# Optimization experiments

Measured on AMD Instinct MI355X. Metric: run time of the kernel, lower is better.

## Reference

```python
import jax, jax.numpy as jnp
import numpy as np

NEG_SLOPE = 0.1

def lrelu(x):
    return jnp.where(x >= 0, x, NEG_SLOPE * x)

def conv1d(x, w, b, stride=2):
    # x: [N, C_in, W], w: [C_out, C_in, K], VALID padding, given stride
    y = jax.lax.conv_general_dilated(x, w, (stride,), 'VALID',
                                     dimension_numbers=('NCH', 'OIH', 'NCH'))
    return y + b[None, :, None]

def setup_inputs() -> dict:
    key = jax.random.key(0)
    ks = jax.random.split(key, 16)
    N_NODES = 50000
    N_EDGES = 4950000
    POS_C, CONV_C, CONV_W = 3, 3, 151
    HID, OUT = 256, 1
    W2 = 37  # width after two stride-2 k=3 convs on 151
    IN_G = POS_C + W2  # 40

    def lin_init(k, fan_out, fan_in):
        s = 1.0 / np.sqrt(fan_in)
        k1, k2 = jax.random.split(k)
        return (jax.random.uniform(k1, (fan_out, fan_in), jnp.float32, -s, s),
                jax.random.uniform(k2, (fan_out,), jnp.float32, -s, s))

    pose = jax.random.normal(ks[0], (N_NODES, POS_C), jnp.float32)
    views = jax.random.normal(ks[1], (N_NODES, CONV_C, CONV_W), jnp.float32)
    edge_index = jax.random.randint(ks[2], (2, N_EDGES), 0, N_NODES, jnp.int64)

    # encoder1: Conv1d(3 -> 9, k=3, s=2); encoder2: Conv1d(9 -> 1, k=3, s=2)
    s1 = 1.0 / np.sqrt(CONV_C * 3)
    w_e1 = jax.random.uniform(ks[3], (CONV_C ** 2, CONV_C, 3), jnp.float32, -s1, s1)
    b_e1 = jax.random.uniform(ks[4], (CONV_C ** 2,), jnp.float32, -s1, s1)
    s2 = 1.0 / np.sqrt(CONV_C ** 2 * 3)
    w_e2 = jax.random.uniform(ks[5], (1, CONV_C ** 2, 3), jnp.float32, -s2, s2)
    b_e2 = jax.random.uniform(ks[6], (1,), jnp.float32, -s2, s2)

    # GraphConv: lin_rel (with bias) on aggregated neighbors, lin_root (no bias) on self
    w_rel, b_rel = lin_init(ks[7], HID, IN_G)
    w_root, _ = lin_init(ks[8], HID, IN_G)

    w_l1, b_l1 = lin_init(ks[9], HID, HID)
    w_l2, b_l2 = lin_init(ks[10], HID, HID)
    w_l3, b_l3 = lin_init(ks[11], HID, HID)
    w_pred, b_pred = lin_init(ks[12], OUT, HID)

    return dict(pose=pose, views=views, edge_index=edge_index,
                w_e1=w_e1, b_e1=b_e1, w_e2=w_e2, b_e2=b_e2,
                w_rel=w_rel, b_rel=b_rel, w_root=w_root,
                w_l1=w_l1, b_l1=b_l1, w_l2=w_l2, b_l2=b_l2,
                w_l3=w_l3, b_l3=b_l3, w_pred=w_pred, b_pred=b_pred)

def reference(pose, views, edge_index, w_e1, b_e1, w_e2, b_e2,
              w_rel, b_rel, w_root,
              w_l1, b_l1, w_l2, b_l2, w_l3, b_l3, w_pred, b_pred):
    n_nodes = pose.shape[0]
    # view encoder
    v = lrelu(conv1d(views, w_e1, b_e1))          # [N, 9, 75]
    v = lrelu(conv1d(v, w_e2, b_e2))              # [N, 1, 37]
    x = jnp.concatenate([pose, v[:, 0, :]], axis=1)  # [N, 40]
    # GraphConv (aggr='add'): out = lin_rel(sum_{j->i} x_j) + lin_root(x_i)
    src, dst = edge_index[0], edge_index[1]
    agg = jax.ops.segment_sum(x[src], dst, num_segments=n_nodes)  # [N, 40]
    h = lrelu(agg @ w_rel.T + b_rel + x @ w_root.T)               # [N, 256]
    # MLP stack (dropout is identity in eval mode)
    h = lrelu(h @ w_l1.T + b_l1)
    h = lrelu(h @ w_l2.T + b_l2)
    h = lrelu(h @ w_l3.T + b_l3)
    return h @ w_pred.T + b_pred  # [N, 1]
```

## Files before the change

### kernel.cpp

```cpp
#include <hip/hip_runtime.h>
#include <hip/hip_fp16.h>

#define NEG_SLOPE 0.1f
__device__ __forceinline__ float lrelu(float v) { return fmaxf(v, NEG_SLOPE * v); }

constexpr int CAP = 8704;
constexpr int EPB = 8192;

typedef __attribute__((ext_vector_type(8))) short short8;
typedef __attribute__((ext_vector_type(4))) float f32x4;

__device__ __forceinline__ unsigned short f2bf(float f) {
    union { float f; unsigned u; } v; v.f = f;
    const unsigned r = v.u + 0x7FFF + ((v.u >> 16) & 1);
    return (unsigned short)(r >> 16);
}
__device__ __forceinline__ float bf2f(unsigned short h) {
    union { unsigned u; float f; } v; v.u = ((unsigned)h) << 16;
    return v.f;
}

__global__ __launch_bounds__(256) void encoder_kernel(
        const float* __restrict__ pose,
        const float* __restrict__ views,
        const float* __restrict__ w1, const float* __restrict__ b1,
        const float* __restrict__ w2, const float* __restrict__ b2,
        const float* __restrict__ w_l1, const float* __restrict__ w_l2,
        const float* __restrict__ w_l3, const float* __restrict__ w_rel,
        const float* __restrict__ w_root,
        unsigned short* __restrict__ Wb1, unsigned short* __restrict__ Wb2,
        unsigned short* __restrict__ Wb3, unsigned short* __restrict__ Wg,
        int* __restrict__ gcur,
        unsigned short* __restrict__ xHi, unsigned short* __restrict__ xLo,
        __half* __restrict__ xh, int N)
{
    __shared__ float s_w1[81];
    __shared__ float s_b1[9];
    __shared__ float s_w2[27];
    __shared__ float s_b2[1];
    __shared__ float s_c1[4][9][80];

    const int t = threadIdx.x;

    if (blockIdx.x < 256) {
        const int i = blockIdx.x * 256 + t;
        Wb1[i] = f2bf(w_l1[i]);
        Wb2[i] = f2bf(w_l2[i]);
        Wb3[i] = f2bf(w_l3[i]);
        if (i < 40960) {
            const int m = i / 160, c = i % 160;
            const int k = c % 80;
            const float v = (k < 40) ? w_rel[m * 40 + k] : w_root[m * 40 + (k - 40)];
            Wg[i] = f2bf(v);
        }
        if (i < 1024) gcur[i] = 0;
        if (i < 40) xh[(size_t)N * 40 + i] = __float2half(0.f);
    }

    if (t < 81) s_w1[t] = w1[t];
    if (t >= 96 && t < 105) s_b1[t - 96] = b1[t - 96];
    if (t >= 128 && t < 155) s_w2[t - 128] = w2[t - 128];
    if (t == 240) s_b2[0] = b2[0];
    __syncthreads();

    const int nb = blockIdx.x * 4;

    #pragma unroll
    for (int pass = 0; pass < 2; pass++) {
        const int task = pass * 256 + t;
        if (task < 300) {
            const int ln = task / 75;
            const int p  = task % 75;
            const int n  = min(nb + ln, N - 1);
            const float* __restrict__ vin = views + (size_t)n * 453 + 2 * p;
            float e[3], o[3], e1[3];
            #pragma unroll
            for (int ic = 0; ic < 3; ic++) {
                const float* ci = vin + ic * 151;
                e[ic] = ci[0]; o[ic] = ci[1]; e1[ic] = ci[2];
            }
            const int didx = (p & 1) * 40 + (p >> 1);
            #pragma unroll
            for (int oc = 0; oc < 9; oc++) {
                float v = s_b1[oc];
                #pragma unroll
                for (int ic = 0; ic < 3; ic++)
                    v += s_w1[oc * 9 + ic * 3 + 0] * e[ic]
                       + s_w1[oc * 9 + ic * 3 + 1] * o[ic]
                       + s_w1[oc * 9 + ic * 3 + 2] * e1[ic];
                s_c1[ln][oc][didx] = lrelu(v);
            }
        }
    }
    __syncthreads();

    if (t < 160) {
        const int ln = t / 40, f = t % 40;
        const int n  = min(nb + ln, N - 1);
        float outv;
        if (f < 3) {
            outv = pose[(size_t)n * 3 + f];
        } else {
            const int ow = f - 3;
            float v = s_b2[0];
            #pragma unroll
            for (int ic = 0; ic < 9; ic++)
                v += s_w2[ic * 3 + 0] * s_c1[ln][ic][ow]
                   + s_w2[ic * 3 + 1] * s_c1[ln][ic][40 + ow]
                   + s_w2[ic * 3 + 2] * s_c1[ln][ic][ow + 1];
            outv = lrelu(v);
        }
        const unsigned short hi = f2bf(outv);
        const unsigned short lo = f2bf(outv - bf2f(hi));
        xHi[(size_t)n * 40 + f] = hi;
        xLo[(size_t)n * 40 + f] = lo;
        xh[(size_t)n * 40 + f] = __float2half(outv);
    }
}

__global__ __launch_bounds__(512) void bin_kernel(
        const int* __restrict__ ei, int* __restrict__ gcur,
        int* __restrict__ pairs, int E, int NB)
{
    __shared__ int s_hist[1024];
    __shared__ int s_loff[1024];
    __shared__ int s_base[1024];
    __shared__ int s_wave8[8];
    __shared__ int s_pk[EPB];
    __shared__ unsigned short s_bkt[EPB];
    const int t = threadIdx.x;
    const int lane = t & 63, wid = t >> 6;
    const int e0 = blockIdx.x * EPB + t * 16;
    const int tot = min(E - (int)blockIdx.x * EPB, EPB);

    for (int i = t; i < 1024; i += 512) s_hist[i] = 0;
    __syncthreads();

    int pk[16], mt[16];
    auto proc = [&](int j, int sv, int dv) {
        const int b = dv >> 6;
        const int r = atomicAdd(&s_hist[b], 1);
        pk[j] = sv * 80 | ((dv & 63) << 22);
        mt[j] = b | (r << 10);
    };

    if (e0 + 16 <= E) {
        #pragma unroll
        for (int q = 0; q < 4; q++) {
            const int4 sv = *(const int4*)(ei + e0 + 4 * q);
            const int4 dv = *(const int4*)(ei + E + e0 + 4 * q);
            proc(4 * q + 0, sv.x, dv.x);
            proc(4 * q + 1, sv.y, dv.y);
            proc(4 * q + 2, sv.z, dv.z);
            proc(4 * q + 3, sv.w, dv.w);
        }
    } else {
        #pragma unroll
        for (int j = 0; j < 16; j++) {
            mt[j] = -1;
            const int e = e0 + j;
            if (e < E) proc(j, ei[e], ei[E + e]);
        }
    }
    __syncthreads();

    int carry = 0;
    #pragma unroll
    for (int base = 0; base < 1024; base += 512) {
        const int i = base + t;
        const int v = s_hist[i];
        int sc = v;
        #pragma unroll
        for (int d = 1; d < 64; d <<= 1) {
            const int u = __shfl_up(sc, d);
            if (lane >= d) sc += u;
        }
        if (lane == 63) s_wave8[wid] = sc;
        __syncthreads();
        if (wid == 0) {
            int wv = (lane < 8) ? s_wave8[lane] : 0;
            #pragma unroll
            for (int d = 1; d < 8; d <<= 1) {
                const int u = __shfl_up(wv, d);
                if (lane >= d) wv += u;
            }
            if (lane < 8) s_wave8[lane] = wv;
        }
        __syncthreads();
        const int waveoff = (wid > 0) ? s_wave8[wid - 1] : 0;
        s_loff[i] = carry + waveoff + sc - v;
        const int chunk_tot = s_wave8[7];
        __syncthreads();
        carry += chunk_tot;
    }

    for (int i = t; i < NB; i += 512) {
        const int c = s_hist[i];
        if (c > 0) s_base[i] = atomicAdd(&gcur[i], c);
    }
    __syncthreads();

    #pragma unroll
    for (int j = 0; j < 16; j++) {
        if (mt[j] >= 0) {
            const int b = mt[j] & 1023;
            const int pos = s_loff[b] + (mt[j] >> 10);
            s_pk[pos] = pk[j];
            s_bkt[pos] = (unsigned short)b;
        }
    }
    __syncthreads();

    for (int i = t; i < tot; i += 512) {
        const int b = s_bkt[i];
        const int p = s_base[b] + (i - s_loff[b]);
        if (p < CAP) pairs[b * CAP + p] = s_pk[i];
    }
}

__global__ __launch_bounds__(512) void sort_gather_kernel(
        const int* __restrict__ gcur,
        const int* __restrict__ pairs,
        const __half* __restrict__ xh,
        unsigned short* __restrict__ aggHi,
        unsigned short* __restrict__ aggLo, int N)
{
    __shared__ int s_sorted[CAP];
    __shared__ int s_cnt[64], s_off[64], s_cur[64];
    const int b = blockIdx.x;
    const int t = threadIdx.x;
    const int cnt = min(gcur[b], CAP);
    const int* __restrict__ pr = pairs + (size_t)b * CAP;

    if (t < 64) s_cnt[t] = 0;

    int pk[17];
    #pragma unroll
    for (int j = 0; j < 17; j++) {
        const int i = t + j * 512;
        pk[j] = (i < cnt) ? __builtin_nontemporal_load(pr + i) : -1;
    }
    __syncthreads();

    #pragma unroll
    for (int j = 0; j < 17; j++)
        if (pk[j] >= 0) atomicAdd(&s_cnt[pk[j] >> 22], 1);
    __syncthreads();

    if (t < 64) {
        const int c = s_cnt[t];
        const int p = ((c + 23) / 24) * 24;
        int sc = p;
        #pragma unroll
        for (int d = 1; d < 64; d <<= 1) {
            const int u = __shfl_up(sc, d);
            if (t >= d) sc += u;
        }
        const int excl = sc - p;
        s_off[t] = excl;
        s_cur[t] = excl;
    }
    __syncthreads();

    if (t < 64) {
        const int e0 = s_off[t] + s_cnt[t];
        const int e1 = s_off[t] + ((s_cnt[t] + 23) / 24) * 24;
        for (int i = e0; i < e1 && i < CAP; i++) s_sorted[i] = N * 80;
    }
    #pragma unroll
    for (int j = 0; j < 17; j++) {
        if (pk[j] >= 0) {
            const int pos = atomicAdd(&s_cur[pk[j] >> 22], 1);
            if (pos < CAP) s_sorted[pos] = pk[j] & 0x3FFFFF;
        }
    }
    __syncthreads();

    const int wave = t >> 6, lane = t & 63;
    const int slot = min(lane / 5, 11);
    const int f8 = lane % 5;
    const char* __restrict__ xb = (const char*)xh + f8 * 16;

    #pragma unroll 1
    for (int i = 0; i < 8; i++) {
        const int ln = wave * 8 + i;
        const int n = b * 64 + ln;
        if (n >= N) break;
        const int c = s_cnt[ln];
        const int cntp = ((c + 23) / 24) * 24;
        const int* __restrict__ srt = s_sorted + s_off[ln] + slot;

        float a[8];
        #pragma unroll
        for (int j = 0; j < 8; j++) a[j] = 0.f;

        union { unsigned v; __half2 h; } cv;
        float2 f;
        auto acc8 = [&](uint4 u) {
            cv.v = u.x; f = __half22float2(cv.h); a[0] += f.x; a[1] += f.y;
            cv.v = u.y; f = __half22float2(cv.h); a[2] += f.x; a[3] += f.y;
            cv.v = u.z; f = __half22float2(cv.h); a[4] += f.x; a[5] += f.y;
            cv.v = u.w; f = __half22float2(cv.h); a[6] += f.x; a[7] += f.y;
        };

        int e = 0;
        #pragma unroll 1
        for (; e + 48 <= cntp; e += 48) {
            const int o0 = srt[e];
            const int o1 = srt[e + 12];
            const int o2 = srt[e + 24];
            const int o3 = srt[e + 36];
            const uint4 u0 = *(const uint4*)(xb + o0);
            const uint4 u1 = *(const uint4*)(xb + o1);
            const uint4 u2 = *(const uint4*)(xb + o2);
            const uint4 u3 = *(const uint4*)(xb + o3);
            acc8(u0); acc8(u1); acc8(u2); acc8(u3);
        }
        if (e < cntp) {
            const int o0 = srt[e];
            const int o1 = srt[e + 12];
            const uint4 u0 = *(const uint4*)(xb + o0);
            const uint4 u1 = *(const uint4*)(xb + o1);
            acc8(u0); acc8(u1);
        }

        #pragma unroll
        for (int j = 0; j < 8; j++) a[j] += __shfl(a[j], lane + 30);
        #pragma unroll
        for (int j = 0; j < 8; j++) a[j] += __shfl(a[j], lane + 15);
        #pragma unroll
        for (int j = 0; j < 8; j++) a[j] += __shfl(a[j], lane + 5) + __shfl(a[j], lane + 10);

        if (lane < 5) {
            unsigned short h[8], l[8];
            #pragma unroll
            for (int j = 0; j < 8; j++) {
                h[j] = f2bf(a[j]);
                l[j] = f2bf(a[j] - bf2f(h[j]));
            }
            uint4 H, L;
            H.x = h[0] | ((unsigned)h[1] << 16); H.y = h[2] | ((unsigned)h[3] << 16);
            H.z = h[4] | ((unsigned)h[5] << 16); H.w = h[6] | ((unsigned)h[7] << 16);
            L.x = l[0] | ((unsigned)l[1] << 16); L.y = l[2] | ((unsigned)l[3] << 16);
            L.z = l[4] | ((unsigned)l[5] << 16); L.w = l[6] | ((unsigned)l[7] << 16);
            *(uint4*)(aggHi + (size_t)n * 40 + lane * 8) = H;
            *(uint4*)(aggLo + (size_t)n * 40 + lane * 8) = L;
        }
    }
}

__device__ __forceinline__ void gemm_tile(const unsigned short* __restrict__ aT,
                                          const unsigned short* __restrict__ W,
                                          int wstride, int K,
                                          int wave, int l16, int q,
                                          f32x4 acc[4][4])
{
    for (int k0 = 0; k0 < K; k0 += 32) {
        short8 af[4], wf[4];
        #pragma unroll
        for (int nt = 0; nt < 4; nt++)
            af[nt] = *(const short8*)(aT + (nt * 16 + l16) * 264 + k0 + q * 8);
        #pragma unroll
        for (int mt = 0; mt < 4; mt++)
            wf[mt] = *(const short8*)(W + (wave * 64 + mt * 16 + l16) * wstride + k0 + q * 8);
        #pragma unroll
        for (int nt = 0; nt < 4; nt++)
            #pragma unroll
            for (int mt = 0; mt < 4; mt++)
                acc[nt][mt] = __builtin_amdgcn_mfma_f32_16x16x32_bf16(af[nt], wf[mt], acc[nt][mt], 0, 0, 0);
    }
}

__device__ __forceinline__ void epi_to_lds(f32x4 acc[4][4], const float* __restrict__ b,
                                           unsigned short* __restrict__ aT,
                                           int wave, int l16, int q)
{
    float bias[4];
    #pragma unroll
    for (int mt = 0; mt < 4; mt++) bias[mt] = b[wave * 64 + mt * 16 + l16];
    #pragma unroll
    for (int nt = 0; nt < 4; nt++)
        #pragma unroll
        for (int r = 0; r < 4; r++)
            #pragma unroll
            for (int mt = 0; mt < 4; mt++) {
                const int row = nt * 16 + q * 4 + r;
                const int col = wave * 64 + mt * 16 + l16;
                aT[row * 264 + col] = f2bf(lrelu(acc[nt][mt][r] + bias[mt]));
            }
}

__global__ void fused_gemm_kernel(const unsigned short* __restrict__ aggHi,
                                  const unsigned short* __restrict__ aggLo,
                                  const unsigned short* __restrict__ xHi,
                                  const unsigned short* __restrict__ xLo,
                                  const unsigned short* __restrict__ Wg,
                                  const float* __restrict__ b_rel,
                                  const unsigned short* __restrict__ Wb1,
                                  const float* __restrict__ b_l1,
                                  const unsigned short* __restrict__ Wb2,
                                  const float* __restrict__ b_l2,
                                  const unsigned short* __restrict__ Wb3,
                                  const float* __restrict__ b_l3,
                                  const float* __restrict__ w_pred,
                                  const float* __restrict__ b_pred,
                                  float* __restrict__ out, int N)
{
    __shared__ __align__(16) unsigned short aT[64 * 264];
    __shared__ float s_part[4][64];
    const int t = threadIdx.x;
    const int n0 = blockIdx.x * 64;
    const int wave = t >> 6, lane = t & 63, q = lane >> 4, l16 = lane & 15;

    for (int u = t; u < 640; u += 256) {
        const int row = u / 10, c = (u % 10) * 4;
        const int srow = min(n0 + row, N - 1);
        const size_t off = (size_t)srow * 40 + c;
        unsigned short* rp = aT + row * 264;
        *(ushort4*)(rp + c)       = *(const ushort4*)(aggHi + off);
        *(ushort4*)(rp + 40 + c)  = *(const ushort4*)(xHi + off);
        *(ushort4*)(rp + 80 + c)  = *(const ushort4*)(aggLo + off);
        *(ushort4*)(rp + 120 + c) = *(const ushort4*)(xLo + off);
    }
    __syncthreads();

    {
        f32x4 acc[4][4] = {};
        gemm_tile(aT, Wg, 160, 160, wave, l16, q, acc);
        __syncthreads();
        epi_to_lds(acc, b_rel, aT, wave, l16, q);
        __syncthreads();
    }
    {
        f32x4 acc[4][4] = {};
        gemm_tile(aT, Wb1, 256, 256, wave, l16, q, acc);
        __syncthreads();
        epi_to_lds(acc, b_l1, aT, wave, l16, q);
        __syncthreads();
    }
    {
        f32x4 acc[4][4] = {};
        gemm_tile(aT, Wb2, 256, 256, wave, l16, q, acc);
        __syncthreads();
        epi_to_lds(acc, b_l2, aT, wave, l16, q);
        __syncthreads();
    }
    {
        f32x4 acc[4][4] = {};
        gemm_tile(aT, Wb3, 256, 256, wave, l16, q, acc);

        float bias[4], wp[4];
        #pragma unroll
        for (int mt = 0; mt < 4; mt++) {
            const int col = wave * 64 + mt * 16 + l16;
            bias[mt] = b_l3[col];
            wp[mt] = w_pred[col];
        }
        #pragma unroll
        for (int nt = 0; nt < 4; nt++)
            #pragma unroll
            for (int r = 0; r < 4; r++) {
                float p = 0.f;
                #pragma unroll
                for (int mt = 0; mt < 4; mt++)
                    p += lrelu(acc[nt][mt][r] + bias[mt]) * wp[mt];
                p += __shfl_xor(p, 1);
                p += __shfl_xor(p, 2);
                p += __shfl_xor(p, 4);
                p += __shfl_xor(p, 8);
                if (l16 == 0) s_part[wave][nt * 16 + q * 4 + r] = p;
            }
        __syncthreads();

        if (t < 64) {
            const int row = n0 + t;
            if (row < N)
                out[row] = s_part[0][t] + s_part[1][t] + s_part[2][t] + s_part[3][t] + b_pred[0];
        }
    }
}

extern "C" void kernel_launch(void* const* d_in, const int* in_sizes, int n_in,
                              void* d_out, int out_size, void* d_ws, size_t ws_size,
                              hipStream_t stream)
{
    const float* pose   = (const float*)d_in[0];
    const float* views  = (const float*)d_in[1];
    const int*   ei     = (const int*)d_in[2];
    const float* w_e1   = (const float*)d_in[3];
    const float* b_e1   = (const float*)d_in[4];
    const float* w_e2   = (const float*)d_in[5];
    const float* b_e2   = (const float*)d_in[6];
    const float* w_rel  = (const float*)d_in[7];
    const float* b_rel  = (const float*)d_in[8];
    const float* w_root = (const float*)d_in[9];
    const float* w_l1   = (const float*)d_in[10];
    const float* b_l1   = (const float*)d_in[11];
    const float* w_l2   = (const float*)d_in[12];
    const float* b_l2   = (const float*)d_in[13];
    const float* w_l3   = (const float*)d_in[14];
    const float* b_l3   = (const float*)d_in[15];
    const float* w_pred = (const float*)d_in[16];
    const float* b_pred = (const float*)d_in[17];
    float* out = (float*)d_out;

    const int N = in_sizes[0] / 3;
    const int E = in_sizes[2] / 2;
    const int NB = (N + 63) >> 6;
    const int NBLK = (N + 63) / 64;

    unsigned short* xHi = (unsigned short*)d_ws;
    unsigned short* xLo = xHi + (size_t)N * 40;
    unsigned short* aggHi = xLo + (size_t)N * 40;
    unsigned short* aggLo = aggHi + (size_t)N * 40;
    __half* xh = (__half*)(aggLo + (size_t)N * 40);
    int* pairs = (int*)(xh + (size_t)(N + 1) * 40 + 24);
    int* gcur  = pairs + (size_t)NB * CAP;
    unsigned short* Wb1 = (unsigned short*)(gcur + 1024);
    unsigned short* Wb2 = Wb1 + 256 * 256;
    unsigned short* Wb3 = Wb2 + 256 * 256;
    unsigned short* Wg  = Wb3 + 256 * 256;

    encoder_kernel<<<(N + 3) / 4, 256, 0, stream>>>(
        pose, views, w_e1, b_e1, w_e2, b_e2,
        w_l1, w_l2, w_l3, w_rel, w_root,
        Wb1, Wb2, Wb3, Wg, gcur, xHi, xLo, xh, N);

    bin_kernel<<<(E + EPB - 1) / EPB, 512, 0, stream>>>(ei, gcur, pairs, E, NB);

    sort_gather_kernel<<<NB, 512, 0, stream>>>(gcur, pairs, xh, aggHi, aggLo, N);

    fused_gemm_kernel<<<NBLK, 256, 0, stream>>>(
        aggHi, aggLo, xHi, xLo, Wg, b_rel,
        Wb1, b_l1, Wb2, b_l2, Wb3, b_l3,
        w_pred, b_pred, out, N);
}
```

Baseline: 333.9 us.

## Double-buffer MLP weight panels in LDS via async global-to-LDS loads

The fused MLP kernel now stages each 32-wide K panel of the weight matrix into LDS using direct global_load_lds instructions, double-buffered so the load of panel p+2 overlaps the MFMAs on panel p. Before, the weights were read straight from global memory into registers on every K step. The activation tile in LDS also switches from a padded 264-element row stride to an XOR-swizzled 256 stride to avoid bank conflicts. The change relies on hand-placed waitcnt and sched_barrier instructions, and it reuses the weight buffer for the final partial sums, which adds ordering risk.

```diff
diff --git a/kernel.cpp b/kernel.cpp
--- a/kernel.cpp
+++ b/kernel.cpp
@@ -349,20 +349,60 @@
     }
 }
 
-__device__ __forceinline__ void gemm_tile(const unsigned short* __restrict__ aT,
-                                          const unsigned short* __restrict__ W,
-                                          int wstride, int K,
-                                          int wave, int l16, int q,
-                                          f32x4 acc[4][4])
-{
-    for (int k0 = 0; k0 < K; k0 += 32) {
+__device__ __forceinline__ int aswz(int row, int col) {
+    return row * 256 + (col ^ ((row & 7) << 3));
+}
+
+__device__ __forceinline__ void gload16(const void* g, void* l) {
+    __builtin_amdgcn_global_load_lds(
+        (const __attribute__((address_space(1))) unsigned int*)g,
+        (__attribute__((address_space(3))) unsigned int*)l,
+        16, 0, 0);
+}
+
+__device__ __forceinline__ void stage_panel(const unsigned short* __restrict__ W,
+                                            int wstride, int k0,
+                                            unsigned short* buf, int wave, int lane)
+{
+    const int rbase = wave * 64 + (lane >> 2);
+    const int cu = (lane & 3) * 8;
+    #pragma unroll
+    for (int j = 0; j < 4; j++) {
+        const int row = rbase + j * 16;
+        gload16(W + (size_t)row * wstride + k0 + cu,
+                buf + (wave * 4 + j) * 512);
+    }
+}
+
+__device__ __forceinline__ void gemm_layer(const unsigned short* __restrict__ aT,
+                                           const unsigned short* __restrict__ W,
+                                           int wstride, int K,
+                                           unsigned short* __restrict__ sW0,
+                                           unsigned short* __restrict__ sW1,
+                                           int wave, int lane, int l16, int q,
+                                           f32x4 acc[4][4])
+{
+    const int NP = K >> 5;
+    stage_panel(W, wstride, 0, sW0, wave, lane);
+    stage_panel(W, wstride, 32, sW1, wave, lane);
+    const int wrow = (wave * 64 + l16) * 32 + q * 8;
+
+    for (int p = 0; p < NP; p++) {
+        unsigned short* wb = (p & 1) ? sW1 : sW0;
+        if (p + 1 < NP) asm volatile("s_waitcnt vmcnt(4)" ::: "memory");
+        else            asm volatile("s_waitcnt vmcnt(0)" ::: "memory");
         short8 af[4], wf[4];
         #pragma unroll
         for (int nt = 0; nt < 4; nt++)
-            af[nt] = *(const short8*)(aT + (nt * 16 + l16) * 264 + k0 + q * 8);
+            af[nt] = *(const short8*)(aT + aswz(nt * 16 + l16, p * 32 + q * 8));
         #pragma unroll
         for (int mt = 0; mt < 4; mt++)
-            wf[mt] = *(const short8*)(W + (wave * 64 + mt * 16 + l16) * wstride + k0 + q * 8);
+            wf[mt] = *(const short8*)(wb + wrow + mt * 16 * 32);
+        if (p + 2 < NP) {
+            asm volatile("s_waitcnt lgkmcnt(0)" ::: "memory");
+            __builtin_amdgcn_sched_barrier(0);
+            stage_panel(W, wstride, (p + 2) * 32, wb, wave, lane);
+        }
         #pragma unroll
         for (int nt = 0; nt < 4; nt++)
             #pragma unroll
@@ -386,11 +426,12 @@
             for (int mt = 0; mt < 4; mt++) {
                 const int row = nt * 16 + q * 4 + r;
                 const int col = wave * 64 + mt * 16 + l16;
-                aT[row * 264 + col] = f2bf(lrelu(acc[nt][mt][r] + bias[mt]));
-            }
-}
-
-__global__ void fused_gemm_kernel(const unsigned short* __restrict__ aggHi,
+                aT[aswz(row, col)] = f2bf(lrelu(acc[nt][mt][r] + bias[mt]));
+            }
+}
+
+__global__ __launch_bounds__(256) void fused_gemm_kernel(
+                                  const unsigned short* __restrict__ aggHi,
                                   const unsigned short* __restrict__ aggLo,
                                   const unsigned short* __restrict__ xHi,
                                   const unsigned short* __restrict__ xLo,
@@ -406,8 +447,8 @@
                                   const float* __restrict__ b_pred,
                                   float* __restrict__ out, int N)
 {
-    __shared__ __align__(16) unsigned short aT[64 * 264];
-    __shared__ float s_part[4][64];
+    __shared__ __align__(16) unsigned short aT[64 * 256];
+    __shared__ __align__(16) unsigned short sW[2][256 * 32];
     const int t = threadIdx.x;
     const int n0 = blockIdx.x * 64;
     const int wave = t >> 6, lane = t & 63, q = lane >> 4, l16 = lane & 15;
@@ -416,38 +457,37 @@
         const int row = u / 10, c = (u % 10) * 4;
         const int srow = min(n0 + row, N - 1);
         const size_t off = (size_t)srow * 40 + c;
-        unsigned short* rp = aT + row * 264;
-        *(ushort4*)(rp + c)       = *(const ushort4*)(aggHi + off);
-        *(ushort4*)(rp + 40 + c)  = *(const ushort4*)(xHi + off);
-        *(ushort4*)(rp + 80 + c)  = *(const ushort4*)(aggLo + off);
-        *(ushort4*)(rp + 120 + c) = *(const ushort4*)(xLo + off);
+        *(ushort4*)(aT + aswz(row, c))       = *(const ushort4*)(aggHi + off);
+        *(ushort4*)(aT + aswz(row, 40 + c))  = *(const ushort4*)(xHi + off);
+        *(ushort4*)(aT + aswz(row, 80 + c))  = *(const ushort4*)(aggLo + off);
+        *(ushort4*)(aT + aswz(row, 120 + c)) = *(const ushort4*)(xLo + off);
     }
     __syncthreads();
 
     {
         f32x4 acc[4][4] = {};
-        gemm_tile(aT, Wg, 160, 160, wave, l16, q, acc);
+        gemm_layer(aT, Wg, 160, 160, sW[0], sW[1], wave, lane, l16, q, acc);
         __syncthreads();
         epi_to_lds(acc, b_rel, aT, wave, l16, q);
         __syncthreads();
     }
     {
         f32x4 acc[4][4] = {};
-        gemm_tile(aT, Wb1, 256, 256, wave, l16, q, acc);
+        gemm_layer(aT, Wb1, 256, 256, sW[0], sW[1], wave, lane, l16, q, acc);
         __syncthreads();
         epi_to_lds(acc, b_l1, aT, wave, l16, q);
         __syncthreads();
     }
     {
         f32x4 acc[4][4] = {};
-        gemm_tile(aT, Wb2, 256, 256, wave, l16, q, acc);
+        gemm_layer(aT, Wb2, 256, 256, sW[0], sW[1], wave, lane, l16, q, acc);
         __syncthreads();
         epi_to_lds(acc, b_l2, aT, wave, l16, q);
         __syncthreads();
     }
     {
         f32x4 acc[4][4] = {};
-        gemm_tile(aT, Wb3, 256, 256, wave, l16, q, acc);
+        gemm_layer(aT, Wb3, 256, 256, sW[0], sW[1], wave, lane, l16, q, acc);
 
         float bias[4], wp[4];
         #pragma unroll
@@ -456,6 +496,7 @@
             bias[mt] = b_l3[col];
             wp[mt] = w_pred[col];
         }
+        float* spw = (float*)(sW[0] + (wave * 4) * 512);
         #pragma unroll
         for (int nt = 0; nt < 4; nt++)
             #pragma unroll
@@ -468,14 +509,19 @@
                 p += __shfl_xor(p, 2);
                 p += __shfl_xor(p, 4);
                 p += __shfl_xor(p, 8);
-                if (l16 == 0) s_part[wave][nt * 16 + q * 4 + r] = p;
+                if (l16 == 0) spw[nt * 16 + q * 4 + r] = p;
             }
         __syncthreads();
 
         if (t < 64) {
             const int row = n0 + t;
-            if (row < N)
-                out[row] = s_part[0][t] + s_part[1][t] + s_part[2][t] + s_part[3][t] + b_pred[0];
+            if (row < N) {
+                float s = b_pred[0];
+                #pragma unroll
+                for (int w = 0; w < 4; w++)
+                    s += ((const float*)(sW[0] + (w * 4) * 512))[t];
+                out[row] = s;
+            }
         }
     }
 }
```

Result: faster. 326.9 us (-2.1%).
